# Kernel tuning notes

Hardware: AMD Instinct MI355X
Metric: run time of the kernel (lower is better)

## Reference

```python
import jax, jax.numpy as jnp
import numpy as np

NUM_HEADS = 16


def setup_inputs() -> dict:
    key = jax.random.key(0)
    ks = jax.random.split(key, 6)
    B, S, D = 2, 2048, 2048
    scale = 0.02
    return {
        "hidden_states": jax.random.normal(ks[0], (B, S, D), dtype=jnp.float32),
        "Wq": jax.random.normal(ks[1], (D, D), dtype=jnp.float32) * scale,
        "Wk": jax.random.normal(ks[2], (D, D), dtype=jnp.float32) * scale,
        "Wv": jax.random.normal(ks[3], (D, D), dtype=jnp.float32) * scale,
        "Wo": jax.random.normal(ks[4], (D, D), dtype=jnp.float32) * scale,
        "bo": jnp.zeros((D,), dtype=jnp.float32),
    }


def reference(hidden_states, Wq, Wk, Wv, Wo, bo):
    B, S, D = hidden_states.shape
    H = NUM_HEADS
    hd = D // H

    def split_heads(t):  # [B,S,D] -> [B,H,S,hd]
        return t.reshape(B, S, H, hd).transpose(0, 2, 1, 3)

    q = split_heads(hidden_states @ Wq)
    k = split_heads(hidden_states @ Wk)
    v = split_heads(hidden_states @ Wv)

    # Note: GPT-Neo does NOT scale by 1/sqrt(head_dim); scores computed in fp32.
    scores = jnp.einsum("bhqd,bhkd->bhqk", q.astype(jnp.float32), k.astype(jnp.float32))
    causal = jnp.tril(jnp.ones((S, S), dtype=bool))  # [S,S], True = attend
    mask_value = jnp.finfo(jnp.float32).min
    scores = jnp.where(causal[None, None, :, :], scores, mask_value)
    attn = jax.nn.softmax(scores, axis=-1).astype(v.dtype)

    ctx = jnp.einsum("bhqk,bhkd->bhqd", attn, v)  # [B,H,S,hd]
    ctx = ctx.transpose(0, 2, 1, 3).reshape(B, S, D)  # merge heads
    out = ctx @ Wo + bo
    return out
```

## Files before the change

### kernel.cpp

```cpp
#include <hip/hip_runtime.h>
#include <hip/hip_bf16.h>
#include <math.h>

#define BATCH 2
#define SEQ   2048
#define DDIM  2048
#define NH    16
#define HD    128
#define MROWS (BATCH * SEQ)

typedef unsigned short u16;
typedef __bf16 bf16x8 __attribute__((ext_vector_type(8)));
typedef float  f32x4  __attribute__((ext_vector_type(4)));
typedef float  f32x16 __attribute__((ext_vector_type(16)));

__device__ __forceinline__ u16 f2bf(float f) {
  unsigned int u = __float_as_uint(f);
  u += 0x7fffu + ((u >> 16) & 1u);
  return (u16)(u >> 16);
}
__device__ __forceinline__ float bf2f(u16 h) {
  return __uint_as_float(((unsigned int)h) << 16);
}

__device__ __forceinline__ void gload16(const void* g, void* s) {
  __builtin_amdgcn_global_load_lds((const __attribute__((address_space(1))) void*)g,
                                   (__attribute__((address_space(3))) void*)s, 16, 0, 0);
}

__global__ void split_x(const float* __restrict__ in, u16* __restrict__ hi,
                        u16* __restrict__ lo) {
  const int i = blockIdx.x * blockDim.x + threadIdx.x;
  float4 v = ((const float4*)in)[i];
  ushort4 h, l;
  h.x = f2bf(v.x); l.x = f2bf(v.x - bf2f(h.x));
  h.y = f2bf(v.y); l.y = f2bf(v.y - bf2f(h.y));
  h.z = f2bf(v.z); l.z = f2bf(v.z - bf2f(h.z));
  h.w = f2bf(v.w); l.w = f2bf(v.w - bf2f(h.w));
  ((ushort4*)hi)[i] = h;
  ((ushort4*)lo)[i] = l;
}

__global__ void transpose_w(const float* __restrict__ W, u16* __restrict__ Wth,
                            u16* __restrict__ Wtl) {
  __shared__ float t[32][33];
  const int tx = threadIdx.x, ty = threadIdx.y;
  const int c0 = blockIdx.x * 32, r0 = blockIdx.y * 32;
#pragma unroll
  for (int i = 0; i < 4; ++i)
    t[ty + i * 8][tx] = W[(size_t)(r0 + ty + i * 8) * DDIM + c0 + tx];
  __syncthreads();
#pragma unroll
  for (int i = 0; i < 4; ++i) {
    const float v = t[tx][ty + i * 8];
    const u16 h = f2bf(v);
    const size_t idx = (size_t)(c0 + ty + i * 8) * DDIM + r0 + tx;
    Wth[idx] = h;
    if (Wtl) Wtl[idx] = f2bf(v - bf2f(h));
  }
}

__global__ void transpose_v(const u16* __restrict__ V, u16* __restrict__ Vt) {
  __shared__ u16 t[32][33];
  const int tx = threadIdx.x, ty = threadIdx.y;
  const int s0 = blockIdx.x * 32;
  const int d0 = blockIdx.y * 32;
  const int bh = blockIdx.z;
  const int b = bh >> 4, h = bh & 15;
#pragma unroll
  for (int i = 0; i < 4; ++i)
    t[ty + i * 8][tx] = V[(size_t)(b * SEQ + s0 + ty + i * 8) * DDIM + h * HD + d0 + tx];
  __syncthreads();
#pragma unroll
  for (int i = 0; i < 4; ++i)
    Vt[((size_t)bh * HD + d0 + ty + i * 8) * SEQ + s0 + tx] = t[tx][ty + i * 8];
}

template <int MODE>
__global__ __launch_bounds__(256)
void gemm_kernel(const u16* __restrict__ A, const u16* __restrict__ Bt,
                 void* __restrict__ Cout, const float* __restrict__ bias) {
  constexpr int K = DDIM, N = DDIM;
  __shared__ __align__(16) u16 As[128 * 64];
  __shared__ __align__(16) u16 Bs[128 * 64];
  const int tid = threadIdx.x;
  const int wave = tid >> 6;
  const int lane = tid & 63;
  const int lr = lane & 15, lg = lane >> 4;
  const int bm = blockIdx.y * 128, bn = blockIdx.x * 128;
  const int wr = wave >> 1, wc = wave & 1;

  f32x4 acc[4][4] = {};

  const int srow = wave * 32 + (lane >> 3);
  const int scol = (lane & 7) * 8;
  const u16* Ag = A  + (size_t)(bm + srow) * K + scol;
  const u16* Bg = Bt + (size_t)(bn + srow) * K + scol;

  for (int k0 = 0; k0 < K; k0 += 64) {
    __syncthreads();
#pragma unroll
    for (int it = 0; it < 4; ++it) {
      gload16(Ag + (size_t)it * 8 * K + k0, &As[(wave * 32 + it * 8) * 64]);
      gload16(Bg + (size_t)it * 8 * K + k0, &Bs[(wave * 32 + it * 8) * 64]);
    }
    __syncthreads();
#pragma unroll
    for (int kk = 0; kk < 64; kk += 32) {
      bf16x8 af[4], bfr[4];
#pragma unroll
      for (int i = 0; i < 4; ++i)
        af[i] = *(const bf16x8*)&As[(wr * 64 + i * 16 + lr) * 64 + kk + lg * 8];
#pragma unroll
      for (int j = 0; j < 4; ++j)
        bfr[j] = *(const bf16x8*)&Bs[(wc * 64 + j * 16 + lr) * 64 + kk + lg * 8];
#pragma unroll
      for (int i = 0; i < 4; ++i)
#pragma unroll
        for (int j = 0; j < 4; ++j)
          acc[i][j] = __builtin_amdgcn_mfma_f32_16x16x32_bf16(af[i], bfr[j], acc[i][j], 0, 0, 0);
    }
  }

#pragma unroll
  for (int i = 0; i < 4; ++i) {
    const int row0 = bm + wr * 64 + i * 16 + lg * 4;
#pragma unroll
    for (int j = 0; j < 4; ++j) {
      const int col = bn + wc * 64 + j * 16 + lr;
#pragma unroll
      for (int e = 0; e < 4; ++e) {
        const int row = row0 + e;
        const float v = acc[i][j][e];
        if constexpr (MODE == 0) {
          ((u16*)Cout)[(size_t)row * N + col] = f2bf(v);
        } else {
          ((float*)Cout)[(size_t)row * N + col] = v + bias[col];
        }
      }
    }
  }
}

template <int TERMS, bool WRITE_LO>
__global__ __launch_bounds__(256)
void gemm3_kernel(const u16* __restrict__ Ah, const u16* __restrict__ Al,
                  const u16* __restrict__ Bh, const u16* __restrict__ Bl,
                  u16* __restrict__ Ch, u16* __restrict__ Cl) {
  constexpr int K = DDIM, N = DDIM;
  __shared__ __align__(16) u16 Ash[128 * 64];
  __shared__ __align__(16) u16 Asl[TERMS == 3 ? 128 * 64 : 8];
  __shared__ __align__(16) u16 Bsh[128 * 64];
  __shared__ __align__(16) u16 Bsl[128 * 64];
  const int tid = threadIdx.x;
  const int wave = tid >> 6;
  const int lane = tid & 63;
  const int lr = lane & 15, lg = lane >> 4;
  const int bm = blockIdx.y * 128, bn = blockIdx.x * 128;
  const int wr = wave >> 1, wc = wave & 1;

  f32x4 acc[4][4] = {};

  const int srow = wave * 32 + (lane >> 3);
  const int scol = (lane & 7) * 8;
  const size_t aoff = (size_t)(bm + srow) * K + scol;
  const size_t boff = (size_t)(bn + srow) * K + scol;

  for (int k0 = 0; k0 < K; k0 += 64) {
    __syncthreads();
#pragma unroll
    for (int it = 0; it < 4; ++it) {
      const size_t ro = (size_t)it * 8 * K + k0;
      const int ls = (wave * 32 + it * 8) * 64;
      gload16(Ah + aoff + ro, &Ash[ls]);
      if constexpr (TERMS == 3) gload16(Al + aoff + ro, &Asl[ls]);
      gload16(Bh + boff + ro, &Bsh[ls]);
      gload16(Bl + boff + ro, &Bsl[ls]);
    }
    __syncthreads();
#pragma unroll
    for (int kk = 0; kk < 64; kk += 32) {
      bf16x8 ah[4], al[4], bh[4], bl[4];
#pragma unroll
      for (int i = 0; i < 4; ++i) {
        const int off = (wr * 64 + i * 16 + lr) * 64 + kk + lg * 8;
        ah[i] = *(const bf16x8*)&Ash[off];
        if constexpr (TERMS == 3) al[i] = *(const bf16x8*)&Asl[off];
      }
#pragma unroll
      for (int j = 0; j < 4; ++j) {
        const int off = (wc * 64 + j * 16 + lr) * 64 + kk + lg * 8;
        bh[j] = *(const bf16x8*)&Bsh[off];
        bl[j] = *(const bf16x8*)&Bsl[off];
      }
#pragma unroll
      for (int i = 0; i < 4; ++i)
#pragma unroll
        for (int j = 0; j < 4; ++j) {
          acc[i][j] = __builtin_amdgcn_mfma_f32_16x16x32_bf16(ah[i], bh[j], acc[i][j], 0, 0, 0);
          acc[i][j] = __builtin_amdgcn_mfma_f32_16x16x32_bf16(ah[i], bl[j], acc[i][j], 0, 0, 0);
          if constexpr (TERMS == 3)
            acc[i][j] = __builtin_amdgcn_mfma_f32_16x16x32_bf16(al[i], bh[j], acc[i][j], 0, 0, 0);
        }
    }
  }

#pragma unroll
  for (int i = 0; i < 4; ++i) {
    const int row0 = bm + wr * 64 + i * 16 + lg * 4;
#pragma unroll
    for (int j = 0; j < 4; ++j) {
      const int col = bn + wc * 64 + j * 16 + lr;
#pragma unroll
      for (int e = 0; e < 4; ++e) {
        const float v = acc[i][j][e];
        const u16 h = f2bf(v);
        const size_t idx = (size_t)(row0 + e) * N + col;
        Ch[idx] = h;
        if constexpr (WRITE_LO) Cl[idx] = f2bf(v - bf2f(h));
      }
    }
  }
}

__global__ __launch_bounds__(256, 1)
void attn_kernel(const u16* __restrict__ Qh, const u16* __restrict__ Khp,
                 const u16* __restrict__ Klp, const u16* __restrict__ Vt,
                 u16* __restrict__ ctx) {
  __shared__ __align__(16) u16 Ksh[2][64 * 128];
  __shared__ __align__(16) u16 Ksl[2][64 * 128];
  __shared__ __align__(16) u16 Vs [2][128 * 64];
  const int tid = threadIdx.x;
  const int wave = tid >> 6, lane = tid & 63;
  const int lq = lane & 31;
  const int hi = lane >> 5;
  const float NEG_INF = -__builtin_inff();

  const int id = blockIdx.x;
  const int xcd = id & 7;
  const int j = id >> 3;
  const int bh = xcd * 4 + (j >> 4);
  const int qb = 15 - (j & 15);
  const int q0 = qb * 128;
  const int b = bh >> 4, h = bh & 15;
  const int qw0 = q0 + wave * 32;

  const u16* Kg = Khp + (size_t)b * SEQ * DDIM + h * HD;
  const u16* Lg = Klp + (size_t)b * SEQ * DDIM + h * HD;
  const u16* Vg = Vt + (size_t)bh * HD * SEQ;

  bf16x8 qf[8];
#pragma unroll
  for (int ks = 0; ks < 8; ++ks)
    qf[ks] = *(const bf16x8*)&Qh[(size_t)(b * SEQ + qw0 + lq) * DDIM + h * HD + ks * 16 + hi * 8];

  const int krow0 = wave * 4 + (lane >> 4);
  const int kcolb = (lane & 15) << 4;
  const int vrow0 = wave * 8 + (lane >> 3);
  const int vcolb = (lane & 7) << 4;

  auto STAGE = [&](int buf, int t) {
    const int kbase = t * 64;
#pragma unroll
    for (int it = 0; it < 4; ++it) {
      const int r = it * 16 + krow0;
      const int c = (kcolb ^ ((r & 7) << 4)) >> 1;
      const size_t g = (size_t)(kbase + r) * DDIM + c;
      gload16(Kg + g, &Ksh[buf][(it * 16 + wave * 4) * 128]);
      gload16(Lg + g, &Ksl[buf][(it * 16 + wave * 4) * 128]);
    }
#pragma unroll
    for (int it = 0; it < 4; ++it) {
      const int d = it * 32 + vrow0;
      const int c = (vcolb ^ ((d & 7) << 4)) >> 1;
      gload16(Vg + (size_t)d * SEQ + kbase + c, &Vs[buf][(it * 32 + wave * 8) * 64]);
    }
  };

  float m = NEG_INF, l = 0.f;
  f32x16 o[4] = {};

  const int nt = 2 * qb + 2;
  int cur = 0;
  STAGE(0, 0);
  __syncthreads();

  for (int t = 0; t < nt; ++t) {
    if (t + 1 < nt) STAGE(cur ^ 1, t + 1);
#pragma unroll
    for (int ks2 = 0; ks2 < 2; ++ks2) {
      const int k0 = t * 64 + ks2 * 32;
      if (k0 <= qw0 + 31) {
        f32x16 s = {};
        __builtin_amdgcn_s_setprio(1);
#pragma unroll
        for (int d8 = 0; d8 < 8; ++d8) {
          const int krow = ks2 * 32 + lq;
          const int cb = ((d8 * 32 + hi * 16) ^ ((krow & 7) << 4)) >> 1;
          bf16x8 kfh = *(const bf16x8*)&Ksh[cur][krow * 128 + cb];
          s = __builtin_amdgcn_mfma_f32_32x32x16_bf16(kfh, qf[d8], s, 0, 0, 0);
          bf16x8 kfl = *(const bf16x8*)&Ksl[cur][krow * 128 + cb];
          s = __builtin_amdgcn_mfma_f32_32x32x16_bf16(kfl, qf[d8], s, 0, 0, 0);
        }
        __builtin_amdgcn_s_setprio(0);
        if (k0 + 31 > qw0) {
          const int qrow = qw0 + lq;
#pragma unroll
          for (int r = 0; r < 16; ++r) {
            const int key = k0 + (r & 3) + 8 * (r >> 2) + 4 * hi;
            if (key > qrow) s[r] = NEG_INF;
          }
        }
        float rm = s[0];
#pragma unroll
        for (int r = 1; r < 16; ++r) rm = fmaxf(rm, s[r]);
        rm = fmaxf(rm, __shfl_xor(rm, 32));
        if (!__all(rm - m <= 8.0f)) {
          const float mn = fmaxf(m, rm);
          const float al = __expf(m - mn);
#pragma unroll
          for (int db = 0; db < 4; ++db)
#pragma unroll
            for (int r = 0; r < 16; ++r) o[db][r] *= al;
          l *= al;
          m = mn;
        }
        float ps[16];
        float ls = 0.f;
#pragma unroll
        for (int r = 0; r < 16; ++r) { ps[r] = __expf(s[r] - m); ls += ps[r]; }
        l += ls + __shfl_xor(ls, 32);
        unsigned pk[8], sw[8];
#pragma unroll
        for (int jj = 0; jj < 8; ++jj) {
          pk[jj] = (unsigned)f2bf(ps[2 * jj]) | ((unsigned)f2bf(ps[2 * jj + 1]) << 16);
          sw[jj] = __shfl_xor(pk[jj], 32);
        }
        __builtin_amdgcn_s_setprio(1);
#pragma unroll
        for (int ksl = 0; ksl < 2; ++ksl) {
          union { unsigned u[4]; bf16x8 v; } pb;
          pb.u[0] = hi ? sw[4 * ksl + 2] : pk[4 * ksl + 0];
          pb.u[1] = hi ? sw[4 * ksl + 3] : pk[4 * ksl + 1];
          pb.u[2] = hi ? pk[4 * ksl + 2] : sw[4 * ksl + 0];
          pb.u[3] = hi ? pk[4 * ksl + 3] : sw[4 * ksl + 1];
#pragma unroll
          for (int db = 0; db < 4; ++db) {
            const int d = db * 32 + lq;
            const int cb = ((ks2 * 64 + ksl * 32 + hi * 16) ^ ((d & 7) << 4)) >> 1;
            bf16x8 vf = *(const bf16x8*)&Vs[cur][d * 64 + cb];
            o[db] = __builtin_amdgcn_mfma_f32_32x32x16_bf16(vf, pb.v, o[db], 0, 0, 0);
          }
        }
        __builtin_amdgcn_s_setprio(0);
      }
    }
    __syncthreads();
    cur ^= 1;
  }

  u16* sm = (u16*)&Vs[0][0] + wave * 4096;
#pragma unroll
  for (int db = 0; db < 4; ++db)
#pragma unroll
    for (int jj = 0; jj < 8; ++jj) {
      const int d0 = db * 32 + 8 * (jj >> 1) + 4 * hi + 2 * (jj & 1);
      const unsigned w = (unsigned)f2bf(o[db][2 * jj] / l) |
                         ((unsigned)f2bf(o[db][2 * jj + 1] / l) << 16);
      *(unsigned*)&sm[((lq * 256 + d0 * 2) ^ ((lq & 7) << 4)) >> 1] = w;
    }
  __builtin_amdgcn_wave_barrier();
  {
    const int qr = lane >> 1, hb = lane & 1;
    const size_t rowbase = (size_t)(b * SEQ + qw0 + qr) * DDIM + h * HD + hb * 64;
#pragma unroll
    for (int c = 0; c < 8; ++c) {
      const int byte = (qr * 256 + hb * 128 + c * 16) ^ ((qr & 7) << 4);
      bf16x8 vv = *(const bf16x8*)&sm[byte >> 1];
      *(bf16x8*)&ctx[rowbase + c * 8] = vv;
    }
  }
}

extern "C" void kernel_launch(void* const* d_in, const int* in_sizes, int n_in,
                              void* d_out, int out_size, void* d_ws, size_t ws_size,
                              hipStream_t stream) {
  const float* X  = (const float*)d_in[0];
  const float* Wq = (const float*)d_in[1];
  const float* Wk = (const float*)d_in[2];
  const float* Wv = (const float*)d_in[3];
  const float* Wo = (const float*)d_in[4];
  const float* bo = (const float*)d_in[5];
  float* out = (float*)d_out;

  const size_t SZ_XD = (size_t)MROWS * DDIM * 2;
  const size_t SZ_W  = (size_t)DDIM * DDIM * 2;

  char* p = (char*)d_ws;
  auto alloc = [&](size_t bytes) {
    char* r = p;
    p += (bytes + 255) & ~(size_t)255;
    return r;
  };
  u16* Xh  = (u16*)alloc(SZ_XD);
  u16* Xl  = (u16*)alloc(SZ_XD);
  u16* Wbh = (u16*)alloc(SZ_W);
  u16* Wbl = (u16*)alloc(SZ_W);
  u16* Qh  = (u16*)alloc(SZ_XD);
  u16* Kh  = (u16*)alloc(SZ_XD);
  u16* Kl  = (u16*)alloc(SZ_XD);
  u16* Vb  = (u16*)alloc(SZ_XD);
  u16* Vt  = Xh;
  u16* ctx = Qh;

  split_x<<<(MROWS * DDIM) / 1024, 256, 0, stream>>>(X, Xh, Xl);

  dim3 tb(32, 8);
  dim3 gg(DDIM / 128, MROWS / 128);

  transpose_w<<<dim3(64, 64), tb, 0, stream>>>(Wq, Wbh, Wbl);
  gemm3_kernel<2, false><<<gg, 256, 0, stream>>>(Xh, Xl, Wbh, Wbl, Qh, nullptr);

  transpose_w<<<dim3(64, 64), tb, 0, stream>>>(Wk, Wbh, Wbl);
  gemm3_kernel<3, true><<<gg, 256, 0, stream>>>(Xh, Xl, Wbh, Wbl, Kh, Kl);

  transpose_w<<<dim3(64, 64), tb, 0, stream>>>(Wv, Wbh, nullptr);
  gemm_kernel<0><<<gg, 256, 0, stream>>>(Xh, Wbh, Vb, nullptr);

  transpose_v<<<dim3(SEQ / 32, HD / 32, BATCH * NH), tb, 0, stream>>>(Vb, Vt);

  transpose_w<<<dim3(64, 64), tb, 0, stream>>>(Wo, Wbh, nullptr);

  attn_kernel<<<512, 256, 0, stream>>>(Qh, Kh, Kl, Vt, ctx);

  gemm_kernel<2><<<gg, 256, 0, stream>>>(ctx, Wbh, out, bo);
}
```

Before: 597.5 us.

## Single-buffer V in attention, raise occupancy, split K/V staging waits, swizzle GEMM tiles

The attention kernel now keeps V in a single shared buffer and double-buffers only K. This cuts LDS use so launch_bounds can allow two blocks per CU. K and V loads are issued at different points in the loop, with explicit vmcnt waits and raw s_barriers in place of __syncthreads, so V can arrive while QK^T and softmax run. The hi/lo K MFMAs now accumulate into two independent chains, and the GEMM kernels remap block IDs so tiles on the same XCD share A and B rows for L2 reuse. The hand-counted vmcnt waits are fragile and risk races if the outstanding-load count does not match the assumed value.

New measurement: 537.9 us. 1.11x faster.

```diff
diff --git a/kernel.cpp b/kernel.cpp
--- a/kernel.cpp
+++ b/kernel.cpp
@@ -76,6 +76,13 @@
     Vt[((size_t)bh * HD + d0 + ty + i * 8) * SEQ + s0 + tx] = t[tx][ty + i * 8];
 }
 
+__device__ __forceinline__ void gemm_tile_swz(int& bm, int& bn) {
+  const int idb = blockIdx.y * 16 + blockIdx.x;
+  const int xcd = idb & 7, jj = idb >> 3;
+  bn = (((xcd & 1) << 3) + (jj >> 3)) * 128;
+  bm = (((xcd >> 1) << 3) + (jj & 7)) * 128;
+}
+
 template <int MODE>
 __global__ __launch_bounds__(256)
 void gemm_kernel(const u16* __restrict__ A, const u16* __restrict__ Bt,
@@ -87,7 +94,8 @@
   const int wave = tid >> 6;
   const int lane = tid & 63;
   const int lr = lane & 15, lg = lane >> 4;
-  const int bm = blockIdx.y * 128, bn = blockIdx.x * 128;
+  int bm, bn;
+  gemm_tile_swz(bm, bn);
   const int wr = wave >> 1, wc = wave & 1;
 
   f32x4 acc[4][4] = {};
@@ -156,7 +164,8 @@
   const int wave = tid >> 6;
   const int lane = tid & 63;
   const int lr = lane & 15, lg = lane >> 4;
-  const int bm = blockIdx.y * 128, bn = blockIdx.x * 128;
+  int bm, bn;
+  gemm_tile_swz(bm, bn);
   const int wr = wave >> 1, wc = wave & 1;
 
   f32x4 acc[4][4] = {};
@@ -223,13 +232,13 @@
   }
 }
 
-__global__ __launch_bounds__(256, 1)
+__global__ __launch_bounds__(256, 2)
 void attn_kernel(const u16* __restrict__ Qh, const u16* __restrict__ Khp,
                  const u16* __restrict__ Klp, const u16* __restrict__ Vt,
                  u16* __restrict__ ctx) {
   __shared__ __align__(16) u16 Ksh[2][64 * 128];
   __shared__ __align__(16) u16 Ksl[2][64 * 128];
-  __shared__ __align__(16) u16 Vs [2][128 * 64];
+  __shared__ __align__(16) u16 Vs[128 * 64];
   const int tid = threadIdx.x;
   const int wave = tid >> 6, lane = tid & 63;
   const int lq = lane & 31;
@@ -249,60 +258,76 @@
   const u16* Lg = Klp + (size_t)b * SEQ * DDIM + h * HD;
   const u16* Vg = Vt + (size_t)bh * HD * SEQ;
 
+  const int krow0 = wave * 4 + (lane >> 4);
+  const int kc = (((lane & 15) << 4) ^ ((krow0 & 7) << 4)) >> 1;
+  const int vrow0 = wave * 8 + (lane >> 3);
+  const int vc = (((lane & 7) << 4) ^ ((vrow0 & 7) << 4)) >> 1;
+  size_t koff[4], voff[4];
+#pragma unroll
+  for (int it = 0; it < 4; ++it) {
+    koff[it] = (size_t)(it * 16 + krow0) * DDIM + kc;
+    voff[it] = (size_t)(it * 32 + vrow0) * SEQ + vc;
+  }
+
+  auto STAGE_K = [&](int buf, int t) {
+    const size_t tb = (size_t)t * 64 * DDIM;
+#pragma unroll
+    for (int it = 0; it < 4; ++it) {
+      gload16(Kg + tb + koff[it], &Ksh[buf][(it * 16 + wave * 4) * 128]);
+      gload16(Lg + tb + koff[it], &Ksl[buf][(it * 16 + wave * 4) * 128]);
+    }
+  };
+  auto STAGE_V = [&](int t) {
+    const size_t tb = (size_t)t * 64;
+#pragma unroll
+    for (int it = 0; it < 4; ++it)
+      gload16(Vg + tb + voff[it], &Vs[(it * 32 + wave * 8) * 64]);
+  };
+
+  STAGE_K(0, 0);
   bf16x8 qf[8];
 #pragma unroll
   for (int ks = 0; ks < 8; ++ks)
     qf[ks] = *(const bf16x8*)&Qh[(size_t)(b * SEQ + qw0 + lq) * DDIM + h * HD + ks * 16 + hi * 8];
 
-  const int krow0 = wave * 4 + (lane >> 4);
-  const int kcolb = (lane & 15) << 4;
-  const int vrow0 = wave * 8 + (lane >> 3);
-  const int vcolb = (lane & 7) << 4;
-
-  auto STAGE = [&](int buf, int t) {
-    const int kbase = t * 64;
-#pragma unroll
-    for (int it = 0; it < 4; ++it) {
-      const int r = it * 16 + krow0;
-      const int c = (kcolb ^ ((r & 7) << 4)) >> 1;
-      const size_t g = (size_t)(kbase + r) * DDIM + c;
-      gload16(Kg + g, &Ksh[buf][(it * 16 + wave * 4) * 128]);
-      gload16(Lg + g, &Ksl[buf][(it * 16 + wave * 4) * 128]);
-    }
-#pragma unroll
-    for (int it = 0; it < 4; ++it) {
-      const int d = it * 32 + vrow0;
-      const int c = (vcolb ^ ((d & 7) << 4)) >> 1;
-      gload16(Vg + (size_t)d * SEQ + kbase + c, &Vs[buf][(it * 32 + wave * 8) * 64]);
-    }
-  };
-
   float m = NEG_INF, l = 0.f;
   f32x16 o[4] = {};
 
   const int nt = 2 * qb + 2;
   int cur = 0;
-  STAGE(0, 0);
-  __syncthreads();
 
   for (int t = 0; t < nt; ++t) {
-    if (t + 1 < nt) STAGE(cur ^ 1, t + 1);
+    STAGE_V(t);
+    const bool more = (t + 1 < nt);
+    if (more) {
+      STAGE_K(cur ^ 1, t + 1);
+      asm volatile("s_waitcnt vmcnt(12)" ::: "memory");
+    } else {
+      asm volatile("s_waitcnt vmcnt(4)" ::: "memory");
+    }
+    __builtin_amdgcn_s_barrier();
+    __builtin_amdgcn_sched_barrier(0);
+
 #pragma unroll
     for (int ks2 = 0; ks2 < 2; ++ks2) {
       const int k0 = t * 64 + ks2 * 32;
-      if (k0 <= qw0 + 31) {
-        f32x16 s = {};
+      const bool act = (k0 <= qw0 + 31);
+      unsigned pk[8];
+      if (act) {
+        f32x16 s1 = {}, s2 = {};
+        const int krow = ks2 * 32 + lq;
+        const int swz = (krow & 7) << 4;
         __builtin_amdgcn_s_setprio(1);
 #pragma unroll
         for (int d8 = 0; d8 < 8; ++d8) {
-          const int krow = ks2 * 32 + lq;
-          const int cb = ((d8 * 32 + hi * 16) ^ ((krow & 7) << 4)) >> 1;
+          const int cb = ((d8 * 32 + hi * 16) ^ swz) >> 1;
           bf16x8 kfh = *(const bf16x8*)&Ksh[cur][krow * 128 + cb];
-          s = __builtin_amdgcn_mfma_f32_32x32x16_bf16(kfh, qf[d8], s, 0, 0, 0);
+          s1 = __builtin_amdgcn_mfma_f32_32x32x16_bf16(kfh, qf[d8], s1, 0, 0, 0);
           bf16x8 kfl = *(const bf16x8*)&Ksl[cur][krow * 128 + cb];
-          s = __builtin_amdgcn_mfma_f32_32x32x16_bf16(kfl, qf[d8], s, 0, 0, 0);
+          s2 = __builtin_amdgcn_mfma_f32_32x32x16_bf16(kfl, qf[d8], s2, 0, 0, 0);
         }
         __builtin_amdgcn_s_setprio(0);
+        f32x16 s = s1 + s2;
         if (k0 + 31 > qw0) {
           const int qrow = qw0 + lq;
 #pragma unroll
@@ -330,12 +355,20 @@
 #pragma unroll
         for (int r = 0; r < 16; ++r) { ps[r] = __expf(s[r] - m); ls += ps[r]; }
         l += ls + __shfl_xor(ls, 32);
-        unsigned pk[8], sw[8];
-#pragma unroll
-        for (int jj = 0; jj < 8; ++jj) {
+#pragma unroll
+        for (int jj = 0; jj < 8; ++jj)
           pk[jj] = (unsigned)f2bf(ps[2 * jj]) | ((unsigned)f2bf(ps[2 * jj + 1]) << 16);
-          sw[jj] = __shfl_xor(pk[jj], 32);
-        }
+      }
+      if (ks2 == 0) {
+        if (more) asm volatile("s_waitcnt vmcnt(8)" ::: "memory");
+        else      asm volatile("s_waitcnt vmcnt(0)" ::: "memory");
+        __builtin_amdgcn_s_barrier();
+        __builtin_amdgcn_sched_barrier(0);
+      }
+      if (act) {
+        unsigned sw[8];
+#pragma unroll
+        for (int jj = 0; jj < 8; ++jj) sw[jj] = __shfl_xor(pk[jj], 32);
         __builtin_amdgcn_s_setprio(1);
 #pragma unroll
         for (int ksl = 0; ksl < 2; ++ksl) {
@@ -348,18 +381,19 @@
           for (int db = 0; db < 4; ++db) {
             const int d = db * 32 + lq;
             const int cb = ((ks2 * 64 + ksl * 32 + hi * 16) ^ ((d & 7) << 4)) >> 1;
-            bf16x8 vf = *(const bf16x8*)&Vs[cur][d * 64 + cb];
+            bf16x8 vf = *(const bf16x8*)&Vs[d * 64 + cb];
             o[db] = __builtin_amdgcn_mfma_f32_32x32x16_bf16(vf, pb.v, o[db], 0, 0, 0);
           }
         }
         __builtin_amdgcn_s_setprio(0);
       }
     }
-    __syncthreads();
+    __builtin_amdgcn_s_barrier();
+    __builtin_amdgcn_sched_barrier(0);
     cur ^= 1;
   }
 
-  u16* sm = (u16*)&Vs[0][0] + wave * 4096;
+  u16* sm = (u16*)Ksh + wave * 4096;
 #pragma unroll
   for (int db = 0; db < 4; ++db)
 #pragma unroll
```
